# Optimization experiments

Hardware: AMD Instinct MI355X
Metric: run time of the kernel (lower is better)

Reference implementation:

```python
import jax, jax.numpy as jnp
import numpy as np

INPUT_DIM = 512
OUTPUT_DIM = 2048
GAMMA = 0.5
N_ROWS = 65536


def setup_inputs() -> dict:
    key = jax.random.key(0)
    kx, kw, kb = jax.random.split(key, 3)
    input_tensor = jax.random.normal(kx, (N_ROWS, INPUT_DIM), dtype=jnp.float32)
    # RBFSampler.fit: random_weights_ = sqrt(2*gamma) * N(0,1), random_offset_ ~ U(0, 2pi)
    W = jnp.sqrt(2.0 * GAMMA) * jax.random.normal(kw, (INPUT_DIM, OUTPUT_DIM), dtype=jnp.float32)
    b = jax.random.uniform(kb, (OUTPUT_DIM,), dtype=jnp.float32, minval=0.0, maxval=2.0 * np.pi)
    return {"input_tensor": input_tensor, "W": W, "b": b}


def reference(input_tensor, W, b):
    # RBFSampler.transform: cos(X @ W + b) * sqrt(2 / n_components)
    proj = input_tensor @ W + b  # [N, output_dim]
    scale = jnp.sqrt(jnp.asarray(2.0 / OUTPUT_DIM, dtype=proj.dtype))
    return jnp.cos(proj) * scale
```

## Files before the change

kernel.cpp:

```cpp
#include <hip/hip_runtime.h>

typedef __bf16 bf16x8 __attribute__((ext_vector_type(8)));
typedef float  f32x4  __attribute__((ext_vector_type(4)));
typedef int    i32x4  __attribute__((ext_vector_type(4)));
typedef char   c16    __attribute__((ext_vector_type(16)));

constexpr int M_ROWS = 65536;
constexpr int N_COLS = 2048;
constexpr int K_DIM  = 512;
constexpr int NKQ    = 8;
constexpr int MBQ    = 512;
constexpr int NBQ    = 16;

constexpr size_t AQ_OFF  = (65536 + 2048) * 4;
constexpr size_t AQ_SZ   = (size_t)MBQ * NKQ * 16384;
constexpr size_t WQ_OFF  = AQ_OFF + AQ_SZ;
constexpr size_t WQ_SZ   = (size_t)NBQ * NKQ * 16384;
constexpr size_t NEEDQ   = WQ_OFF + WQ_SZ;

__device__ __forceinline__ unsigned short f2bf(float f){
  unsigned int u = __float_as_uint(f);
  u += 0x7FFFu + ((u >> 16) & 1u);
  return (unsigned short)(u >> 16);
}
__device__ __forceinline__ float bf2f(unsigned short h){
  return __uint_as_float(((unsigned int)h) << 16);
}
__device__ __forceinline__ void split4(const float4& v, ushort4& h, ushort4& l){
  h.x = f2bf(v.x); l.x = f2bf(v.x - bf2f(h.x));
  h.y = f2bf(v.y); l.y = f2bf(v.y - bf2f(h.y));
  h.z = f2bf(v.z); l.z = f2bf(v.z - bf2f(h.z));
  h.w = f2bf(v.w); l.w = f2bf(v.w - bf2f(h.w));
}

__device__ __forceinline__ void gl_lds16(const void* g, void* l){
  __builtin_amdgcn_global_load_lds(
      (const __attribute__((address_space(1))) unsigned int*)g,
      (__attribute__((address_space(3))) unsigned int*)l, 16, 0, 0);
}

constexpr float INV2PI = 0.15915494309189535f;
__device__ __forceinline__ float cos_scaled(float v){
  float rev = v * INV2PI;
  rev -= floorf(rev);
  return 0.03125f * __builtin_amdgcn_cosf(rev);
}

__device__ __forceinline__ void q2(float x, float inv, char& o1, char& o2){
  float t1 = x * inv;
  float r1 = rintf(t1);
  float r2 = fminf(rintf((t1 - r1) * 256.0f), 127.0f);
  o1 = (char)(int)r1;
  o2 = (char)(int)r2;
}

__global__ void pack_xq(const float* __restrict__ X, char* __restrict__ AQ,
                        float* __restrict__ sXo){
  const int bid = blockIdx.x;
  const int t = threadIdx.x;
  const int rl = t >> 3, seg = t & 7;
  const int grow = bid * 32 + rl;
  const float* src = X + (size_t)grow * K_DIM + seg * 64;
  f32x4 v[16];
  #pragma unroll
  for (int i = 0; i < 16; ++i)
    v[i] = __builtin_nontemporal_load(reinterpret_cast<const f32x4*>(src) + i);
  float m = 0.f;
  #pragma unroll
  for (int i = 0; i < 16; ++i)
    m = fmaxf(m, fmaxf(fmaxf(fabsf(v[i].x), fabsf(v[i].y)),
                       fmaxf(fabsf(v[i].z), fabsf(v[i].w))));
  m = fmaxf(m, __shfl_xor(m, 1));
  m = fmaxf(m, __shfl_xor(m, 2));
  m = fmaxf(m, __shfl_xor(m, 4));
  m = fmaxf(m, 1e-10f);
  if (seg == 0) sXo[grow] = m * (1.0f / 127.0f);
  const float inv = 127.0f / m;

  const int mb = bid >> 2;
  const int rowt = (bid & 3) * 32 + rl;
  const int i_ = rowt >> 4, r_ = rowt & 15;
  char* tb = AQ + (size_t)(mb * NKQ + seg) * 16384;
  #pragma unroll
  for (int q = 0; q < 4; ++q){
    c16 o1, o2;
    #pragma unroll
    for (int u = 0; u < 4; ++u){
      f32x4 xv = v[q * 4 + u];
      #pragma unroll
      for (int w = 0; w < 4; ++w){
        char a, b; q2(xv[w], inv, a, b);
        o1[u * 4 + w] = a; o2[u * 4 + w] = b;
      }
    }
    int c = i_ * 64 + q * 16 + r_;
    *reinterpret_cast<c16*>(tb + c * 16)        = o1;
    *reinterpret_cast<c16*>(tb + 8192 + c * 16) = o2;
  }
}

__global__ void scale_w(const float* __restrict__ W, float* __restrict__ sWo){
  __shared__ float red[8][32];
  int t = threadIdx.x, nl = t & 31, kq = t >> 5;
  int n = blockIdx.x * 32 + nl;
  float m = 0.f;
  for (int k = kq * 64; k < kq * 64 + 64; ++k)
    m = fmaxf(m, fabsf(W[(size_t)k * N_COLS + n]));
  red[kq][nl] = m;
  __syncthreads();
  if (kq == 0){
    #pragma unroll
    for (int u = 1; u < 8; ++u) m = fmaxf(m, red[u][nl]);
    sWo[n] = fmaxf(m, 1e-10f) * (1.0f / 127.0f);
  }
}

__global__ void pack_wq(const float* __restrict__ W, const float* __restrict__ sW,
                        char* __restrict__ WQ){
  __shared__ float tf[64][132];
  const int nb = blockIdx.x, kt = blockIdx.y, t = threadIdx.x;
  const int kr = t >> 2, nq = t & 3;
  #pragma unroll
  for (int it = 0; it < 8; ++it){
    f32x4 v4 = *reinterpret_cast<const f32x4*>(
        W + (size_t)(kt * 64 + kr) * N_COLS + nb * 128 + nq * 32 + it * 4);
    *reinterpret_cast<f32x4*>(&tf[kr][nq * 32 + it * 4]) = v4;
  }
  __syncthreads();
  char* tb = WQ + (size_t)(nb * NKQ + kt) * 16384;
  #pragma unroll
  for (int cc = 0; cc < 2; ++cc){
    int c = t + cc * 256;
    int jj = c >> 6, q = (c >> 4) & 3, fc = c & 15;
    int col_local = (jj >> 2) * 64 + fc * 4 + (jj & 3);
    float inv = 1.0f / sW[nb * 128 + col_local];
    c16 o1, o2;
    #pragma unroll
    for (int e = 0; e < 16; ++e){
      char a, b; q2(tf[q * 16 + e][col_local], inv, a, b);
      o1[e] = a; o2[e] = b;
    }
    *reinterpret_cast<c16*>(tb + c * 16)        = o1;
    *reinterpret_cast<c16*>(tb + 8192 + c * 16) = o2;
  }
}

#define MFMAI(a,b,c) __builtin_amdgcn_mfma_i32_16x16x64_i8(a,b,c,0,0,0)
#define DRAIN_BAR() { asm volatile("s_waitcnt vmcnt(0)" ::: "memory"); \
                      __builtin_amdgcn_sched_barrier(0); __syncthreads(); }

__launch_bounds__(256, 4)
__global__ void rbf_gemm_i8(const char* __restrict__ AQ, const char* __restrict__ WQ,
                            const float* __restrict__ sX, const float* __restrict__ sW,
                            const float* __restrict__ bvec, float* __restrict__ out){
  __shared__ __align__(16) char smem[2 * 8192];

  int orig = blockIdx.x;
  int wgid = (orig & 7) * 2048 + (orig >> 3);
  int mb = wgid >> 5, nb2 = wgid & 31;
  int nb = nb2 >> 1, wn2 = nb2 & 1;

  int tid = threadIdx.x, lane = tid & 63, wid = tid >> 6;
  int r = lane & 15, g = lane >> 4;

  const char* abase = AQ + (size_t)mb * NKQ * 16384;
  const char* bbase = WQ + ((size_t)nb * NKQ) * 16384 + wn2 * 4096;
  const int soff = wid * 1024 + lane * 16;
  const int doff = wid * 1024;

  int aoffs[2];
  #pragma unroll
  for (int i = 0; i < 2; ++i) aoffs[i] = (wid * 2 + i) * 1024 + lane * 16;
  int boffs[4];
  #pragma unroll
  for (int j = 0; j < 4; ++j) boffs[j] = j * 1024 + lane * 16;

  i32x4 accm[2][4], accc[2][4];
  #pragma unroll
  for (int i = 0; i < 2; ++i)
    #pragma unroll
    for (int j = 0; j < 4; ++j){
      accm[i][j] = (i32x4){0,0,0,0};
      accc[i][j] = (i32x4){0,0,0,0};
    }

  i32x4 a1A[2], a2A[2], a1B[2], a2B[2];

  #pragma unroll
  for (int i = 0; i < 2; ++i){
    a1A[i] = *reinterpret_cast<const i32x4*>(abase + aoffs[i]);
    a2A[i] = *reinterpret_cast<const i32x4*>(abase + 8192 + aoffs[i]);
  }
  gl_lds16(bbase + soff, smem + doff);
  gl_lds16(bbase + 8192 + soff, smem + 4096 + doff);
  DRAIN_BAR();

  #pragma unroll 1
  for (int kt = 0; kt < NKQ; kt += 2){
    {
      const char* bb = bbase + (size_t)(kt + 1) * 16384;
      gl_lds16(bb + soff, smem + 8192 + doff);
      gl_lds16(bb + 8192 + soff, smem + 12288 + doff);
      const char* ab = abase + (size_t)(kt + 1) * 16384;
      #pragma unroll
      for (int i = 0; i < 2; ++i){
        a1B[i] = *reinterpret_cast<const i32x4*>(ab + aoffs[i]);
        a2B[i] = *reinterpret_cast<const i32x4*>(ab + 8192 + aoffs[i]);
      }
      const char* SB = smem;
      #pragma unroll
      for (int j = 0; j < 4; ++j){
        i32x4 b1 = *reinterpret_cast<const i32x4*>(SB + boffs[j]);
        i32x4 b2 = *reinterpret_cast<const i32x4*>(SB + 4096 + boffs[j]);
        #pragma unroll
        for (int i = 0; i < 2; ++i){
          accm[i][j] = MFMAI(a1A[i], b1, accm[i][j]);
          accc[i][j] = MFMAI(a1A[i], b2, accc[i][j]);
          accc[i][j] = MFMAI(a2A[i], b1, accc[i][j]);
        }
      }
      DRAIN_BAR();
    }
    {
      if (kt + 2 < NKQ){
        const char* bb = bbase + (size_t)(kt + 2) * 16384;
        gl_lds16(bb + soff, smem + doff);
        gl_lds16(bb + 8192 + soff, smem + 4096 + doff);
        const char* ab = abase + (size_t)(kt + 2) * 16384;
        #pragma unroll
        for (int i = 0; i < 2; ++i){
          a1A[i] = *reinterpret_cast<const i32x4*>(ab + aoffs[i]);
          a2A[i] = *reinterpret_cast<const i32x4*>(ab + 8192 + aoffs[i]);
        }
      }
      const char* SB = smem + 8192;
      #pragma unroll
      for (int j = 0; j < 4; ++j){
        i32x4 b1 = *reinterpret_cast<const i32x4*>(SB + boffs[j]);
        i32x4 b2 = *reinterpret_cast<const i32x4*>(SB + 4096 + boffs[j]);
        #pragma unroll
        for (int i = 0; i < 2; ++i){
          accm[i][j] = MFMAI(a1B[i], b1, accm[i][j]);
          accc[i][j] = MFMAI(a1B[i], b2, accc[i][j]);
          accc[i][j] = MFMAI(a2B[i], b1, accc[i][j]);
        }
      }
      DRAIN_BAR();
    }
  }

  int colb = nb2 * 64 + r * 4;
  f32x4 sw4 = *reinterpret_cast<const f32x4*>(sW + colb);
  f32x4 bv  = *reinterpret_cast<const f32x4*>(bvec + colb);
  #pragma unroll
  for (int i = 0; i < 2; ++i){
    int rowb = mb * 128 + wid * 32 + i * 16 + g * 4;
    f32x4 sx4 = *reinterpret_cast<const f32x4*>(sX + rowb);
    #pragma unroll
    for (int p = 0; p < 4; ++p){
      float sx = sx4[p];
      f32x4 o;
      o.x = cos_scaled(fmaf(sx * sw4.x,
              (float)accm[i][0][p] + (float)accc[i][0][p] * 0.00390625f, bv.x));
      o.y = cos_scaled(fmaf(sx * sw4.y,
              (float)accm[i][1][p] + (float)accc[i][1][p] * 0.00390625f, bv.y));
      o.z = cos_scaled(fmaf(sx * sw4.z,
              (float)accm[i][2][p] + (float)accc[i][2][p] * 0.00390625f, bv.z));
      o.w = cos_scaled(fmaf(sx * sw4.w,
              (float)accm[i][3][p] + (float)accc[i][3][p] * 0.00390625f, bv.w));
      __builtin_nontemporal_store(o,
          reinterpret_cast<f32x4*>(out + (size_t)(rowb + p) * N_COLS + colb));
    }
  }
}

#define MFMA_(a,b,c) __builtin_amdgcn_mfma_f32_16x16x32_bf16(a,b,c,0,0,0)
constexpr int LDSK = 40;
constexpr int SEC  = 128 * LDSK;
__launch_bounds__(256, 2)
__global__ void rbf_gemm_nows(const float* __restrict__ X, const float* __restrict__ W,
                              const float* __restrict__ bvec, float* __restrict__ out){
  __shared__ __align__(16) unsigned short smem[4 * SEC];
  int orig = blockIdx.x;
  int wgid = (orig & 7) * (int)(gridDim.x >> 3) + (orig >> 3);
  int mb = wgid >> 4, nb = wgid & 15;
  int m0 = mb * 128, n0 = nb * 128;
  int tid = threadIdx.x, lane = tid & 63, wid = tid >> 6;
  int wm = wid >> 1, wn = wid & 1;
  int r = lane & 15, g = lane >> 4;

  const float* asrc[4]; int alofs[4]; float4 ra[4];
  const float* wsrc[4]; int wnq4[4]; int wkr[4]; float4 rw[4];
  #pragma unroll
  for (int i = 0; i < 4; ++i){
    int c = tid + i * 256;
    int row = c >> 3, q = c & 7;
    asrc[i]  = X + (size_t)(m0 + row) * K_DIM + q * 4;
    alofs[i] = row * LDSK + q * 4;
  }
  #pragma unroll
  for (int i = 0; i < 4; ++i) ra[i] = *reinterpret_cast<const float4*>(asrc[i]);
  #pragma unroll
  for (int i = 0; i < 4; ++i){
    int c = tid + i * 256;
    int kr = c >> 5, nq = c & 31;
    wsrc[i] = W + (size_t)kr * N_COLS + n0 + nq * 4;
    wkr[i] = kr; wnq4[i] = nq * 4;
  }
  #pragma unroll
  for (int i = 0; i < 4; ++i) rw[i] = *reinterpret_cast<const float4*>(wsrc[i]);

  f32x4 acc[4][4];
  #pragma unroll
  for (int i = 0; i < 4; ++i)
    #pragma unroll
    for (int j = 0; j < 4; ++j) acc[i][j] = (f32x4){0.f,0.f,0.f,0.f};

  int aoff[4], boff[4];
  #pragma unroll
  for (int i = 0; i < 4; ++i) aoff[i] = (wm*64 + i*16 + r) * LDSK + g * 8;
  #pragma unroll
  for (int j = 0; j < 4; ++j) boff[j] = (wn*64 + j*16 + r) * LDSK + g * 8;

  #pragma unroll 1
  for (int kt = 0; kt < 16; ++kt){
    __syncthreads();
    #pragma unroll
    for (int i = 0; i < 4; ++i){
      ushort4 h, l;
      split4(ra[i], h, l);
      *reinterpret_cast<ushort4*>(&smem[alofs[i]])       = h;
      *reinterpret_cast<ushort4*>(&smem[SEC + alofs[i]]) = l;
    }
    #pragma unroll
    for (int i = 0; i < 4; ++i){
      float vv[4] = {rw[i].x, rw[i].y, rw[i].z, rw[i].w};
      #pragma unroll
      for (int w2 = 0; w2 < 4; ++w2){
        unsigned short h = f2bf(vv[w2]);
        unsigned short l = f2bf(vv[w2] - bf2f(h));
        int n = wnq4[i] + w2;
        smem[2*SEC + n*LDSK + wkr[i]] = h;
        smem[3*SEC + n*LDSK + wkr[i]] = l;
      }
    }
    if (kt < 15){
      #pragma unroll
      for (int i = 0; i < 4; ++i)
        ra[i] = *reinterpret_cast<const float4*>(asrc[i] + (kt+1)*32);
      #pragma unroll
      for (int i = 0; i < 4; ++i)
        rw[i] = *reinterpret_cast<const float4*>(wsrc[i] + (size_t)(kt+1)*32*N_COLS);
    }
    __syncthreads();
    bf16x8 ah[4], al[4], bh[4], bl[4];
    #pragma unroll
    for (int i = 0; i < 4; ++i){
      ah[i] = *reinterpret_cast<const bf16x8*>(&smem[aoff[i]]);
      al[i] = *reinterpret_cast<const bf16x8*>(&smem[SEC + aoff[i]]);
    }
    #pragma unroll
    for (int j = 0; j < 4; ++j){
      bh[j] = *reinterpret_cast<const bf16x8*>(&smem[2*SEC + boff[j]]);
      bl[j] = *reinterpret_cast<const bf16x8*>(&smem[3*SEC + boff[j]]);
    }
    #pragma unroll
    for (int i = 0; i < 4; ++i){
      #pragma unroll
      for (int j = 0; j < 4; ++j){
        acc[i][j] = MFMA_(ah[i], bh[j], acc[i][j]);
        acc[i][j] = MFMA_(al[i], bh[j], acc[i][j]);
        acc[i][j] = MFMA_(ah[i], bl[j], acc[i][j]);
      }
    }
  }

  float bvv[4];
  #pragma unroll
  for (int j = 0; j < 4; ++j) bvv[j] = bvec[n0 + wn*64 + j*16 + r];
  #pragma unroll
  for (int i = 0; i < 4; ++i){
    #pragma unroll
    for (int j = 0; j < 4; ++j){
      int col = n0 + wn*64 + j*16 + r;
      #pragma unroll
      for (int p = 0; p < 4; ++p){
        int row = m0 + wm*64 + i*16 + g*4 + p;
        out[(size_t)row * N_COLS + col] = cos_scaled(acc[i][j][p] + bvv[j]);
      }
    }
  }
}

extern "C" void kernel_launch(void* const* d_in, const int* in_sizes, int n_in,
                              void* d_out, int out_size, void* d_ws, size_t ws_size,
                              hipStream_t stream){
  const float* X = (const float*)d_in[0];
  const float* W = (const float*)d_in[1];
  const float* b = (const float*)d_in[2];
  float* out = (float*)d_out;
  char* ws = (char*)d_ws;

  if (ws && ws_size >= NEEDQ){
    float* sX = (float*)ws;
    float* sW = (float*)(ws + 65536 * 4);
    char*  AQ = ws + AQ_OFF;
    char*  WQ = ws + WQ_OFF;
    pack_xq<<<2048, 256, 0, stream>>>(X, AQ, sX);
    scale_w<<<64, 256, 0, stream>>>(W, sW);
    pack_wq<<<dim3(NBQ, NKQ), 256, 0, stream>>>(W, sW, WQ);
    rbf_gemm_i8<<<16384, 256, 0, stream>>>(AQ, WQ, sX, sW, b, out);
  } else {
    rbf_gemm_nows<<<8192, 256, 0, stream>>>(X, W, b, out);
  }
}
```

Baseline: 311.2 us.

## Merge W scale and pack kernels; relax GEMM barriers to partial vmcnt waits

After: 357.5 us. +14.9%, slower.

```diff
diff --git a/kernel.cpp b/kernel.cpp
--- a/kernel.cpp
+++ b/kernel.cpp
@@ -99,55 +99,63 @@
   }
 }
 
-__global__ void scale_w(const float* __restrict__ W, float* __restrict__ sWo){
-  __shared__ float red[8][32];
-  int t = threadIdx.x, nl = t & 31, kq = t >> 5;
-  int n = blockIdx.x * 32 + nl;
-  float m = 0.f;
-  for (int k = kq * 64; k < kq * 64 + 64; ++k)
-    m = fmaxf(m, fabsf(W[(size_t)k * N_COLS + n]));
-  red[kq][nl] = m;
-  __syncthreads();
-  if (kq == 0){
-    #pragma unroll
-    for (int u = 1; u < 8; ++u) m = fmaxf(m, red[u][nl]);
-    sWo[n] = fmaxf(m, 1e-10f) * (1.0f / 127.0f);
-  }
-}
-
-__global__ void pack_wq(const float* __restrict__ W, const float* __restrict__ sW,
-                        char* __restrict__ WQ){
+__global__ void prep_w(const float* __restrict__ W, float* __restrict__ sWo,
+                       char* __restrict__ WQ){
   __shared__ float tf[64][132];
-  const int nb = blockIdx.x, kt = blockIdx.y, t = threadIdx.x;
+  __shared__ float sWl[128];
+  const int nb = blockIdx.x, t = threadIdx.x;
+  const int n0 = nb * 128;
+  {
+    int c = t & 127, kh = t >> 7;
+    float m = 0.f;
+    for (int k = kh * 256; k < kh * 256 + 256; ++k)
+      m = fmaxf(m, fabsf(W[(size_t)k * N_COLS + n0 + c]));
+    float* red = reinterpret_cast<float*>(tf);
+    red[kh * 128 + c] = m;
+    __syncthreads();
+    if (t < 128){
+      float mm = fmaxf(fmaxf(red[t], red[128 + t]), 1e-10f) * (1.0f / 127.0f);
+      sWl[t] = mm;
+      sWo[n0 + t] = mm;
+    }
+    __syncthreads();
+  }
   const int kr = t >> 2, nq = t & 3;
-  #pragma unroll
-  for (int it = 0; it < 8; ++it){
-    f32x4 v4 = *reinterpret_cast<const f32x4*>(
-        W + (size_t)(kt * 64 + kr) * N_COLS + nb * 128 + nq * 32 + it * 4);
-    *reinterpret_cast<f32x4*>(&tf[kr][nq * 32 + it * 4]) = v4;
-  }
-  __syncthreads();
-  char* tb = WQ + (size_t)(nb * NKQ + kt) * 16384;
-  #pragma unroll
-  for (int cc = 0; cc < 2; ++cc){
-    int c = t + cc * 256;
-    int jj = c >> 6, q = (c >> 4) & 3, fc = c & 15;
-    int col_local = (jj >> 2) * 64 + fc * 4 + (jj & 3);
-    float inv = 1.0f / sW[nb * 128 + col_local];
-    c16 o1, o2;
-    #pragma unroll
-    for (int e = 0; e < 16; ++e){
-      char a, b; q2(tf[q * 16 + e][col_local], inv, a, b);
-      o1[e] = a; o2[e] = b;
-    }
-    *reinterpret_cast<c16*>(tb + c * 16)        = o1;
-    *reinterpret_cast<c16*>(tb + 8192 + c * 16) = o2;
+  #pragma unroll 1
+  for (int kt = 0; kt < NKQ; ++kt){
+    #pragma unroll
+    for (int it = 0; it < 8; ++it){
+      f32x4 v4 = *reinterpret_cast<const f32x4*>(
+          W + (size_t)(kt * 64 + kr) * N_COLS + n0 + nq * 32 + it * 4);
+      *reinterpret_cast<f32x4*>(&tf[kr][nq * 32 + it * 4]) = v4;
+    }
+    __syncthreads();
+    char* tb = WQ + (size_t)(nb * NKQ + kt) * 16384;
+    #pragma unroll
+    for (int cc = 0; cc < 2; ++cc){
+      int c = t + cc * 256;
+      int jj = c >> 6, q = (c >> 4) & 3, fc = c & 15;
+      int col_local = (jj >> 2) * 64 + fc * 4 + (jj & 3);
+      float inv = 1.0f / sWl[col_local];
+      c16 o1, o2;
+      #pragma unroll
+      for (int e = 0; e < 16; ++e){
+        char a, b; q2(tf[q * 16 + e][col_local], inv, a, b);
+        o1[e] = a; o2[e] = b;
+      }
+      *reinterpret_cast<c16*>(tb + c * 16)        = o1;
+      *reinterpret_cast<c16*>(tb + 8192 + c * 16) = o2;
+    }
+    __syncthreads();
   }
 }
 
 #define MFMAI(a,b,c) __builtin_amdgcn_mfma_i32_16x16x64_i8(a,b,c,0,0,0)
 #define DRAIN_BAR() { asm volatile("s_waitcnt vmcnt(0)" ::: "memory"); \
                       __builtin_amdgcn_sched_barrier(0); __syncthreads(); }
+#define CNT_BAR4() { asm volatile("s_waitcnt vmcnt(4)" ::: "memory"); \
+                     __builtin_amdgcn_s_barrier(); \
+                     __builtin_amdgcn_sched_barrier(0); }
 
 __launch_bounds__(256, 4)
 __global__ void rbf_gemm_i8(const char* __restrict__ AQ, const char* __restrict__ WQ,
@@ -201,6 +209,7 @@
       const char* bb = bbase + (size_t)(kt + 1) * 16384;
       gl_lds16(bb + soff, smem + 8192 + doff);
       gl_lds16(bb + 8192 + soff, smem + 12288 + doff);
+      __builtin_amdgcn_sched_barrier(0);
       const char* ab = abase + (size_t)(kt + 1) * 16384;
       #pragma unroll
       for (int i = 0; i < 2; ++i){
@@ -219,13 +228,14 @@
           accc[i][j] = MFMAI(a2A[i], b1, accc[i][j]);
         }
       }
-      DRAIN_BAR();
+      CNT_BAR4();
     }
     {
       if (kt + 2 < NKQ){
         const char* bb = bbase + (size_t)(kt + 2) * 16384;
         gl_lds16(bb + soff, smem + doff);
         gl_lds16(bb + 8192 + soff, smem + 4096 + doff);
+        __builtin_amdgcn_sched_barrier(0);
         const char* ab = abase + (size_t)(kt + 2) * 16384;
         #pragma unroll
         for (int i = 0; i < 2; ++i){
@@ -245,7 +255,7 @@
           accc[i][j] = MFMAI(a2B[i], b1, accc[i][j]);
         }
       }
-      DRAIN_BAR();
+      CNT_BAR4();
     }
   }
 
@@ -407,8 +417,7 @@
     char*  AQ = ws + AQ_OFF;
     char*  WQ = ws + WQ_OFF;
     pack_xq<<<2048, 256, 0, stream>>>(X, AQ, sX);
-    scale_w<<<64, 256, 0, stream>>>(W, sW);
-    pack_wq<<<dim3(NBQ, NKQ), 256, 0, stream>>>(W, sW, WQ);
+    prep_w<<<NBQ, 256, 0, stream>>>(W, sW, WQ);
     rbf_gemm_i8<<<16384, 256, 0, stream>>>(AQ, WQ, sX, sW, b, out);
   } else {
     rbf_gemm_nows<<<8192, 256, 0, stream>>>(X, W, b, out);
```
